# Performance work log

Hardware: AMD Instinct MI355X
Metric: run time of the kernel (lower is better)

The kernel has to match this reference:

```python
import jax, jax.numpy as jnp
import numpy as np

B, C, H, W = 4, 64, 128, 128
EPS = 1e-5


def setup_inputs() -> dict:
    key = jax.random.key(0)
    ks = jax.random.split(key, 6)
    x = jax.random.normal(ks[0], (B, C, H, W), jnp.float32)
    W1 = jax.random.normal(ks[1], (C, C), jnp.float32) * 0.1
    b1 = jnp.zeros((C,), jnp.float32)
    W2 = jax.random.normal(ks[2], (C, C), jnp.float32) * 0.1
    b2 = jnp.zeros((C,), jnp.float32)
    Wc = jax.random.normal(ks[3], (C, C, 3, 3), jnp.float32) * 0.05
    bn_w = jnp.ones((C,), jnp.float32)
    bn_b = jnp.zeros((C,), jnp.float32)
    gamma = jax.random.normal(ks[4], (1,), jnp.float32) * 0.5
    return dict(x=x, W1=W1, b1=b1, W2=W2, b2=b2, Wc=Wc, bn_w=bn_w, bn_b=bn_b, gamma=gamma)


def reference(x, W1, b1, W2, b2, Wc, bn_w, bn_b, gamma):
    b, c, h, w = x.shape
    # feat_h: [B,W,C,H] flattened to [C, B*W, H] (exact torch .view semantics)
    feat_h = x.transpose(0, 3, 1, 2).reshape(c, b * w, h)
    # feat_w: [B,H,C,W] flattened to [C, B*H, W]
    feat_w = x.transpose(0, 2, 1, 3).reshape(c, b * h, w)
    # avg-pool over W -> [B,C,H] -> [C,H,B]; 1x1 conv == channel mix on dim0
    enc_h = jnp.einsum('oi,ihb->ohb', W1, x.mean(axis=3).transpose(1, 2, 0)) + b1[:, None, None]  # [C,H,B]
    enc_w = jnp.einsum('oi,iwb->owb', W2, x.mean(axis=2).transpose(1, 2, 0)) + b2[:, None, None]  # [C,W,B]
    # energy_h: [C, B*W, B*W]
    energy_h = jnp.matmul(feat_h, jnp.tile(enc_h, (1, 1, w)))
    rel_h = jax.nn.softmax(energy_h, axis=-1)
    aug_h = jnp.matmul(rel_h, feat_h).reshape(b, w, c, h).transpose(0, 2, 3, 1)  # [B,C,H,W]
    # energy_w: [C, B*H, B*H]
    energy_w = jnp.matmul(feat_w, jnp.tile(enc_w, (1, 1, h)))
    rel_w = jax.nn.softmax(energy_w, axis=-1)
    aug_w = jnp.matmul(rel_w, feat_w).reshape(b, h, c, w).transpose(0, 2, 1, 3)  # [B,C,H,W]
    out = gamma * (aug_h + aug_w) + x
    # 3x3 conv (no bias) + BatchNorm2d (training-mode batch stats) + ReLU
    y = jax.lax.conv_general_dilated(out, Wc, (1, 1), 'SAME',
                                     dimension_numbers=('NCHW', 'OIHW', 'NCHW'))
    mean = y.mean(axis=(0, 2, 3), keepdims=True)
    var = y.var(axis=(0, 2, 3), keepdims=True)
    y = (y - mean) * jax.lax.rsqrt(var + EPS)
    y = y * bn_w[None, :, None, None] + bn_b[None, :, None, None]
    return jax.nn.relu(y)
```

## Files before the change

kernel.cpp:

```cpp
#include <hip/hip_runtime.h>
#include <math.h>

#define BDIM 4
#define CDIM 64
#define HDIM 128
#define WDIM 128
#define PLANE (HDIM*WDIM)
#define CHW (CDIM*PLANE)

typedef unsigned short ushort_t;
typedef short short8 __attribute__((ext_vector_type(8)));
typedef float floatx4 __attribute__((ext_vector_type(4)));

__device__ inline unsigned int pack_bf16(float lo, float hi) {
  unsigned int ul = __float_as_uint(lo);
  unsigned int uh = __float_as_uint(hi);
  unsigned int rl = (ul + 0x7FFFu + ((ul >> 16) & 1u)) >> 16;
  unsigned int rh = (uh + 0x7FFFu + ((uh >> 16) & 1u)) >> 16;
  return (rh << 16) | (rl & 0xFFFFu);
}

__global__ __launch_bounds__(256) void k1_T_rowmean(const float* __restrict__ x,
                                                    float* __restrict__ T,
                                                    float* __restrict__ xmw) {
  int bid = blockIdx.x;
  int b = bid >> 7, h = bid & 127;
  int t = threadIdx.x;
  int wid = t >> 6, lane = t & 63;
  const float* xp = x + (size_t)b * CHW + h * WDIM;
  float tr[4] = {0,0,0,0}, ur[4] = {0,0,0,0};
#pragma unroll
  for (int cc = 0; cc < 16; cc++) {
    int c = wid * 16 + cc;
    int k = cc & 3;
    float v0 = xp[c * PLANE + lane];
    float v1 = xp[c * PLANE + lane + 64];
    tr[k] += v0; ur[k] += v1;
    float s = v0 + v1;
#pragma unroll
    for (int off = 32; off; off >>= 1) s += __shfl_xor(s, off);
    if (lane == 0) xmw[(b * CDIM + c) * HDIM + h] = s * (1.f / WDIM);
  }
  __shared__ float4 pt[4][128];
  pt[wid][lane]      = make_float4(tr[0], tr[1], tr[2], tr[3]);
  pt[wid][lane + 64] = make_float4(ur[0], ur[1], ur[2], ur[3]);
  __syncthreads();
  if (t < 128) {
    float4 a = pt[0][t], bb = pt[1][t], cvec = pt[2][t], d = pt[3][t];
    float4 s = make_float4(a.x + bb.x + cvec.x + d.x, a.y + bb.y + cvec.y + d.y,
                           a.z + bb.z + cvec.z + d.z, a.w + bb.w + cvec.w + d.w);
    ((float4*)T)[(b * HDIM + h) * WDIM + t] = s;
  }
}

__global__ void k2_colmean(const float* __restrict__ x, float* __restrict__ xmh) {
  int bid = blockIdx.x;
  int b = bid >> 6, c = bid & 63;
  int t = threadIdx.x;
  int tw = t & 127, th2 = t >> 7;
  const float* xp = x + (size_t)(b * CDIM + c) * PLANE;
  float s = 0.f;
  for (int h = th2 * 64; h < th2 * 64 + 64; h++) s += xp[h * WDIM + tw];
  __shared__ float sh[256];
  sh[t] = s;
  __syncthreads();
  if (t < 128) xmh[(b * CDIM + c) * WDIM + t] = (sh[t] + sh[t + 128]) * (1.f / HDIM);
}

__global__ void k3_enc_groups(const float* __restrict__ W1, const float* __restrict__ bias1,
                              const float* __restrict__ W2, const float* __restrict__ bias2,
                              const float* __restrict__ xmw, const float* __restrict__ xmh,
                              const float* __restrict__ T,
                              float* __restrict__ ench, float* __restrict__ encw,
                              float* __restrict__ Gh, float* __restrict__ Gw) {
  int bid = blockIdx.x;
  int t = threadIdx.x;
  if (bid < 256) {
    int o = t >> 2, bb = t & 3;
    if (bid < HDIM) {
      int h = bid;
      float s = bias1[o];
      for (int i = 0; i < CDIM; i++) s += W1[o * CDIM + i] * xmw[(bb * CDIM + i) * HDIM + h];
      ench[(o * HDIM + h) * 4 + bb] = s;
    } else {
      int w = bid - HDIM;
      float s = bias2[o];
      for (int i = 0; i < CDIM; i++) s += W2[o * CDIM + i] * xmh[(bb * CDIM + i) * WDIM + w];
      encw[(o * WDIM + w) * 4 + bb] = s;
    }
  } else if (t < 128) {
    int c2 = bid - 256;
    int b = c2 >> 4;
    int w0 = (c2 & 15) * 8;
    const float4* T4 = (const float4*)T;
    float4 s = make_float4(0, 0, 0, 0);
#pragma unroll
    for (int dw = 0; dw < 8; dw++) {
      float4 v = T4[(b * HDIM + t) * WDIM + w0 + dw];
      s.x += v.x; s.y += v.y; s.z += v.z; s.w += v.w;
    }
    ((float4*)Gh)[c2 * HDIM + t] = s;
    float4 s2 = make_float4(0, 0, 0, 0);
#pragma unroll
    for (int dh = 0; dh < 8; dh++) {
      float4 v = T4[(b * HDIM + w0 + dh) * WDIM + t];
      s2.x += v.x; s2.y += v.y; s2.z += v.z; s2.w += v.w;
    }
    ((float4*)Gw)[c2 * WDIM + t] = s2;
  }
}

__global__ __launch_bounds__(512) void k4_probs(const float* __restrict__ x,
                                                const float* __restrict__ ench,
                                                const float* __restrict__ encw,
                                                float* __restrict__ Ph,
                                                float* __restrict__ Pw) {
  __shared__ float plane[HDIM * WDIM];
  __shared__ float4 esh[512];
  int bid = blockIdx.x;
  int b = bid >> 6, c = bid & 63;
  int t = threadIdx.x;
  const float* xp = x + (size_t)(b * CDIM + c) * PLANE;
#pragma unroll 4
  for (int j = 0; j < 32; j++) {
    int idx = j * 512 + t;
    int row = idx >> 7, col = idx & 127;
    plane[row * WDIM + (col ^ (row & 31))] = xp[idx];
  }
  __syncthreads();
  int q = t >> 7, p = t & 127;
  int branch = q >> 1, seg = q & 1;
  int c2 = (b * HDIM + p) >> 3;
  float e0 = 0, e1 = 0, e2 = 0, e3 = 0;
  if (branch == 0) {
    const float4* E = (const float4*)ench + c2 * HDIM;
    for (int h = seg * 64; h < seg * 64 + 64; h++) {
      float v = plane[h * WDIM + (p ^ (h & 31))];
      float4 e = E[h];
      e0 += v * e.x; e1 += v * e.y; e2 += v * e.z; e3 += v * e.w;
    }
  } else {
    const float4* E = (const float4*)encw + c2 * WDIM;
    for (int w = seg * 64; w < seg * 64 + 64; w++) {
      float v = plane[p * WDIM + (w ^ (p & 31))];
      float4 e = E[w];
      e0 += v * e.x; e1 += v * e.y; e2 += v * e.z; e3 += v * e.w;
    }
  }
  esh[t] = make_float4(e0, e1, e2, e3);
  __syncthreads();
  if (seg == 0) {
    float4 o = esh[t + 128];
    e0 += o.x; e1 += o.y; e2 += o.z; e3 += o.w;
    float m = fmaxf(fmaxf(e0, e1), fmaxf(e2, e3));
    float p0 = __expf(e0 - m), p1 = __expf(e1 - m), p2 = __expf(e2 - m), p3 = __expf(e3 - m);
    float sc = 1.f / ((p0 + p1 + p2 + p3) * 128.f);
    float4* dst = (branch == 0) ? (float4*)Ph : (float4*)Pw;
    dst[c2 * 512 + (p & 7) * 64 + c] = make_float4(p0 * sc, p1 * sc, p2 * sc, p3 * sc);
  }
}

__global__ void k6_prep(const float* __restrict__ Wc, ushort_t* __restrict__ afrag,
                        float* __restrict__ part) {
  int idx = blockIdx.x * 256 + threadIdx.x;
  if (idx < 128) part[idx] = 0.f;
  if (idx >= 4608) return;
  int lane = idx & 63;
  int m = (idx >> 6) & 3;
  int chunk = (idx >> 8) & 1;
  int tap = idx >> 9;
  int dh = tap / 3, dw = tap % 3;
  int o = m * 16 + (lane & 15);
  int ib = chunk * 32 + (lane >> 4) * 8;
  unsigned int d[4];
#pragma unroll
  for (int j = 0; j < 4; j++) {
    float lo = Wc[((size_t)(o * CDIM + ib + 2 * j) * 3 + dh) * 3 + dw];
    float hi = Wc[((size_t)(o * CDIM + ib + 2 * j + 1) * 3 + dh) * 3 + dw];
    d[j] = pack_bf16(lo, hi);
  }
  uint4* dst = (uint4*)afrag + idx;
  *dst = make_uint4(d[0], d[1], d[2], d[3]);
}

__global__ __launch_bounds__(512) void k6_conv(const float* __restrict__ x,
                                               const float* __restrict__ Ph,
                                               const float* __restrict__ Pw,
                                               const float* __restrict__ Gh,
                                               const float* __restrict__ Gw,
                                               const float* __restrict__ gamma,
                                               const ushort_t* __restrict__ afrag,
                                               float* __restrict__ yb,
                                               float* __restrict__ part) {
  __shared__ uint4 lds_in[3 * 130 * 4];
  __shared__ float sh_s[64], sh_ss[64];
  int bid = blockIdx.x;
  int b = bid >> 7, h0 = bid & 127;
  int t = threadIdx.x;
  int lane = t & 63, wv = t >> 6;
  int w0 = wv * 16;
  const float* xb = x + (size_t)b * CHW;
  const float4* Ph4 = (const float4*)Ph;
  const float4* Pw4 = (const float4*)Pw;
  const float4* Gh4 = (const float4*)Gh;
  const float4* Gw4 = (const float4*)Gw;
  float gm = gamma[0];

  if (t < 64) { sh_s[t] = 0.f; sh_ss[t] = 0.f; }

  floatx4 acc[4];
#pragma unroll
  for (int m = 0; m < 4; m++) acc[m] = (floatx4){0.f, 0.f, 0.f, 0.f};

  for (int chunk = 0; chunk < 2; chunk++) {
    int i0 = chunk * 32;
    __syncthreads();
#pragma unroll
    for (int k = 0; k < 4; k++) {
      int gid = k * 512 + t;
      if (gid < 1560) {
        int wlp = gid % 130;
        int rest = gid / 130;
        int g = rest & 3, lr = rest >> 2;
        int h = h0 - 1 + lr, wl = wlp - 1;
        unsigned int d0 = 0, d1 = 0, d2 = 0, d3 = 0;
        if (h >= 0 && h < HDIM && wl >= 0 && wl < WDIM) {
          int c0 = i0 + g * 8;
          int c2h = (b * HDIM + wl) >> 3;
          int c2w = (b * HDIM + h) >> 3;
          float4 gh4 = Gh4[c2h * HDIM + h];
          float4 gw4 = Gw4[c2w * WDIM + wl];
          const float4* php = Ph4 + c2h * 512 + (wl & 7) * 64 + c0;
          const float4* pwp = Pw4 + c2w * 512 + (h & 7) * 64 + c0;
          const float* xpp = xb + (size_t)c0 * PLANE + h * WDIM + wl;
          float v[8];
#pragma unroll
          for (int j = 0; j < 8; j++) {
            float4 ph = php[j], pw = pwp[j];
            float val = ph.x * gh4.x + ph.y * gh4.y + ph.z * gh4.z + ph.w * gh4.w
                      + pw.x * gw4.x + pw.y * gw4.y + pw.z * gw4.z + pw.w * gw4.w;
            v[j] = fmaf(gm, val, xpp[j * PLANE]);
          }
          d0 = pack_bf16(v[0], v[1]); d1 = pack_bf16(v[2], v[3]);
          d2 = pack_bf16(v[4], v[5]); d3 = pack_bf16(v[6], v[7]);
        }
        int pg = g ^ ((wlp >> 1) & 3);
        lds_in[(lr * 130 + wlp) * 4 + pg] = make_uint4(d0, d1, d2, d3);
      }
    }
    __syncthreads();
#pragma unroll
    for (int tap = 0; tap < 9; tap++) {
      int lr = tap / 3, dw = tap % 3;
      int wlp = w0 + (lane & 15) + dw;
      int pg = (lane >> 4) ^ ((wlp >> 1) & 3);
      short8 bf = *(const short8*)&lds_in[(lr * 130 + wlp) * 4 + pg];
      const short8* ap = (const short8*)afrag + (size_t)((tap * 2 + chunk) * 4) * 64 + lane;
#pragma unroll
      for (int m = 0; m < 4; m++) {
        short8 a = ap[m * 64];
        acc[m] = __builtin_amdgcn_mfma_f32_16x16x32_bf16(a, bf, acc[m], 0, 0, 0);
      }
    }
  }
  int col = lane & 15, rg = lane >> 4;
#pragma unroll
  for (int m = 0; m < 4; m++) {
#pragma unroll
    for (int j = 0; j < 4; j++) {
      int o = m * 16 + rg * 4 + j;
      float v = acc[m][j];
      yb[((size_t)(b * CDIM + o) * HDIM + h0) * WDIM + w0 + col] = v;
      float vs = v, vq = v * v;
#pragma unroll
      for (int off = 1; off < 16; off <<= 1) {
        vs += __shfl_xor(vs, off);
        vq += __shfl_xor(vq, off);
      }
      if (col == 0) {
        atomicAdd(&sh_s[o], vs);
        atomicAdd(&sh_ss[o], vq);
      }
    }
  }
  __syncthreads();
  if (t < 64) {
    atomicAdd(&part[t], sh_s[t]);
    atomicAdd(&part[64 + t], sh_ss[t]);
  }
}

__global__ __launch_bounds__(256) void k8_norm(const float* __restrict__ yb,
                                               const float* __restrict__ part,
                                               const float* __restrict__ bnw,
                                               const float* __restrict__ bnb,
                                               float* __restrict__ out) {
  __shared__ float sa[64], sb2[64];
  int t = threadIdx.x;
  if (t < 64) {
    float s = part[t], ss = part[64 + t];
    float m = s * (1.f / 65536.f);
    float var = ss * (1.f / 65536.f) - m * m;
    float a = rsqrtf(var + 1e-5f) * bnw[t];
    sa[t] = a;
    sb2[t] = bnb[t] - m * a;
  }
  __syncthreads();
  int idx = blockIdx.x * 256 + t;
  int c = (idx >> 12) & 63;
  float4 v = ((const float4*)yb)[idx];
  float a = sa[c], bb = sb2[c];
  v.x = fmaxf(0.f, v.x * a + bb);
  v.y = fmaxf(0.f, v.y * a + bb);
  v.z = fmaxf(0.f, v.z * a + bb);
  v.w = fmaxf(0.f, v.w * a + bb);
  ((float4*)out)[idx] = v;
}

extern "C" void kernel_launch(void* const* d_in, const int* in_sizes, int n_in,
                              void* d_out, int out_size, void* d_ws, size_t ws_size,
                              hipStream_t stream) {
  const float* x     = (const float*)d_in[0];
  const float* W1    = (const float*)d_in[1];
  const float* b1    = (const float*)d_in[2];
  const float* W2    = (const float*)d_in[3];
  const float* b2    = (const float*)d_in[4];
  const float* Wc    = (const float*)d_in[5];
  const float* bnw   = (const float*)d_in[6];
  const float* bnb   = (const float*)d_in[7];
  const float* gamma = (const float*)d_in[8];
  float* out = (float*)d_out;

  float* ws   = (float*)d_ws;
  float* T    = ws;
  float* xmw  = T    + 262144;
  float* xmh  = xmw  + 32768;
  float* ench = xmh  + 32768;
  float* encw = ench + 32768;
  float* Ph   = encw + 32768;
  float* Pw   = Ph   + 131072;
  float* Gh   = Pw   + 131072;
  float* Gw   = Gh   + 32768;
  float* yb   = Gw   + 32768;
  float* part = yb   + 4194304;
  ushort_t* afrag = (ushort_t*)(part + 128);

  k6_prep       <<<18, 256, 0, stream>>>(Wc, afrag, part);
  k1_T_rowmean  <<<512, 256, 0, stream>>>(x, T, xmw);
  k2_colmean    <<<256, 256, 0, stream>>>(x, xmh);
  k3_enc_groups <<<320, 256, 0, stream>>>(W1, b1, W2, b2, xmw, xmh, T, ench, encw, Gh, Gw);
  k4_probs      <<<256, 512, 0, stream>>>(x, ench, encw, Ph, Pw);
  k6_conv       <<<512, 512, 0, stream>>>(x, Ph, Pw, Gh, Gw, gamma, afrag, yb, part);
  k8_norm       <<<4096, 256, 0, stream>>>(yb, part, bnw, bnb, out);
}
```

Before: 186.0 us.

## Split conv rows into half-width blocks and stage all channels at once

The conv kernel now uses 1024 blocks of 256 threads, each covering half a row (64 columns), instead of 512 blocks of 512 threads covering full rows. It loads all 64 input channels into LDS in a single pass, with a single barrier instead of two chunked passes. The Ph vectors are loaded once per column and reused across the three halo rows. The goal is more blocks for occupancy and latency hiding and fewer syncs, at the cost of recomputing halo columns at the block edge and a different LDS swizzle.

```diff
diff --git a/kernel.cpp b/kernel.cpp
--- a/kernel.cpp
+++ b/kernel.cpp
@@ -183,22 +183,22 @@
   *dst = make_uint4(d[0], d[1], d[2], d[3]);
 }
 
-__global__ __launch_bounds__(512) void k6_conv(const float* __restrict__ x,
-                                               const float* __restrict__ Ph,
-                                               const float* __restrict__ Pw,
-                                               const float* __restrict__ Gh,
-                                               const float* __restrict__ Gw,
-                                               const float* __restrict__ gamma,
-                                               const ushort_t* __restrict__ afrag,
-                                               float* __restrict__ yb,
-                                               float* __restrict__ part) {
-  __shared__ uint4 lds_in[3 * 130 * 4];
+__global__ __launch_bounds__(256, 4) void k6_conv(const float* __restrict__ x,
+                                                  const float* __restrict__ Ph,
+                                                  const float* __restrict__ Pw,
+                                                  const float* __restrict__ Gh,
+                                                  const float* __restrict__ Gw,
+                                                  const float* __restrict__ gamma,
+                                                  const ushort_t* __restrict__ afrag,
+                                                  float* __restrict__ yb,
+                                                  float* __restrict__ part) {
+  __shared__ uint4 lds_in[3 * 66 * 8];
   __shared__ float sh_s[64], sh_ss[64];
   int bid = blockIdx.x;
-  int b = bid >> 7, h0 = bid & 127;
+  int wb = bid & 1, h0 = (bid >> 1) & 127, b = bid >> 8;
   int t = threadIdx.x;
   int lane = t & 63, wv = t >> 6;
-  int w0 = wv * 16;
+  int wbase = wb * 64;
   const float* xb = x + (size_t)b * CHW;
   const float4* Ph4 = (const float4*)Ph;
   const float4* Pw4 = (const float4*)Pw;
@@ -208,54 +208,60 @@
 
   if (t < 64) { sh_s[t] = 0.f; sh_ss[t] = 0.f; }
 
+  for (int col = t; col < 528; col += 256) {
+    int g = col / 66;
+    int wlp = col - g * 66;
+    int wl = wbase + wlp - 1;
+    int c0 = g * 8;
+    bool wok = (wl >= 0 && wl < WDIM);
+    float4 ph[8];
+    int c2h = 0;
+    if (wok) {
+      c2h = (b * HDIM + wl) >> 3;
+      const float4* php = Ph4 + c2h * 512 + (wl & 7) * 64 + c0;
+#pragma unroll
+      for (int j = 0; j < 8; j++) ph[j] = php[j];
+    }
+    int pg = g ^ (wlp & 7);
+#pragma unroll
+    for (int lr = 0; lr < 3; lr++) {
+      int h = h0 - 1 + lr;
+      unsigned int d0 = 0, d1 = 0, d2 = 0, d3 = 0;
+      if (wok && h >= 0 && h < HDIM) {
+        int c2w = (b * HDIM + h) >> 3;
+        float4 gh4 = Gh4[c2h * HDIM + h];
+        float4 gw4 = Gw4[c2w * WDIM + wl];
+        const float4* pwp = Pw4 + c2w * 512 + (h & 7) * 64 + c0;
+        const float* xpp = xb + (size_t)c0 * PLANE + h * WDIM + wl;
+        float v[8];
+#pragma unroll
+        for (int j = 0; j < 8; j++) {
+          float4 ph4 = ph[j], pw4 = pwp[j];
+          float val = ph4.x * gh4.x + ph4.y * gh4.y + ph4.z * gh4.z + ph4.w * gh4.w
+                    + pw4.x * gw4.x + pw4.y * gw4.y + pw4.z * gw4.z + pw4.w * gw4.w;
+          v[j] = fmaf(gm, val, xpp[j * PLANE]);
+        }
+        d0 = pack_bf16(v[0], v[1]); d1 = pack_bf16(v[2], v[3]);
+        d2 = pack_bf16(v[4], v[5]); d3 = pack_bf16(v[6], v[7]);
+      }
+      lds_in[(lr * 66 + wlp) * 8 + pg] = make_uint4(d0, d1, d2, d3);
+    }
+  }
+  __syncthreads();
+
   floatx4 acc[4];
 #pragma unroll
   for (int m = 0; m < 4; m++) acc[m] = (floatx4){0.f, 0.f, 0.f, 0.f};
-
-  for (int chunk = 0; chunk < 2; chunk++) {
-    int i0 = chunk * 32;
-    __syncthreads();
-#pragma unroll
-    for (int k = 0; k < 4; k++) {
-      int gid = k * 512 + t;
-      if (gid < 1560) {
-        int wlp = gid % 130;
-        int rest = gid / 130;
-        int g = rest & 3, lr = rest >> 2;
-        int h = h0 - 1 + lr, wl = wlp - 1;
-        unsigned int d0 = 0, d1 = 0, d2 = 0, d3 = 0;
-        if (h >= 0 && h < HDIM && wl >= 0 && wl < WDIM) {
-          int c0 = i0 + g * 8;
-          int c2h = (b * HDIM + wl) >> 3;
-          int c2w = (b * HDIM + h) >> 3;
-          float4 gh4 = Gh4[c2h * HDIM + h];
-          float4 gw4 = Gw4[c2w * WDIM + wl];
-          const float4* php = Ph4 + c2h * 512 + (wl & 7) * 64 + c0;
-          const float4* pwp = Pw4 + c2w * 512 + (h & 7) * 64 + c0;
-          const float* xpp = xb + (size_t)c0 * PLANE + h * WDIM + wl;
-          float v[8];
-#pragma unroll
-          for (int j = 0; j < 8; j++) {
-            float4 ph = php[j], pw = pwp[j];
-            float val = ph.x * gh4.x + ph.y * gh4.y + ph.z * gh4.z + ph.w * gh4.w
-                      + pw.x * gw4.x + pw.y * gw4.y + pw.z * gw4.z + pw.w * gw4.w;
-            v[j] = fmaf(gm, val, xpp[j * PLANE]);
-          }
-          d0 = pack_bf16(v[0], v[1]); d1 = pack_bf16(v[2], v[3]);
-          d2 = pack_bf16(v[4], v[5]); d3 = pack_bf16(v[6], v[7]);
-        }
-        int pg = g ^ ((wlp >> 1) & 3);
-        lds_in[(lr * 130 + wlp) * 4 + pg] = make_uint4(d0, d1, d2, d3);
-      }
-    }
-    __syncthreads();
-#pragma unroll
-    for (int tap = 0; tap < 9; tap++) {
-      int lr = tap / 3, dw = tap % 3;
-      int wlp = w0 + (lane & 15) + dw;
-      int pg = (lane >> 4) ^ ((wlp >> 1) & 3);
-      short8 bf = *(const short8*)&lds_in[(lr * 130 + wlp) * 4 + pg];
-      const short8* ap = (const short8*)afrag + (size_t)((tap * 2 + chunk) * 4) * 64 + lane;
+  int w0loc = wv * 16;
+#pragma unroll
+  for (int tap = 0; tap < 9; tap++) {
+    int lr = tap / 3, dw = tap % 3;
+    int wlp = w0loc + (lane & 15) + dw;
+#pragma unroll
+    for (int kc = 0; kc < 2; kc++) {
+      int pg = (kc * 4 + (lane >> 4)) ^ (wlp & 7);
+      short8 bf = *(const short8*)&lds_in[(lr * 66 + wlp) * 8 + pg];
+      const short8* ap = (const short8*)afrag + (size_t)((tap * 2 + kc) * 4) * 64 + lane;
 #pragma unroll
       for (int m = 0; m < 4; m++) {
         short8 a = ap[m * 64];
@@ -263,6 +269,7 @@
       }
     }
   }
+
   int col = lane & 15, rg = lane >> 4;
 #pragma unroll
   for (int m = 0; m < 4; m++) {
@@ -270,7 +277,7 @@
     for (int j = 0; j < 4; j++) {
       int o = m * 16 + rg * 4 + j;
       float v = acc[m][j];
-      yb[((size_t)(b * CDIM + o) * HDIM + h0) * WDIM + w0 + col] = v;
+      yb[((size_t)(b * CDIM + o) * HDIM + h0) * WDIM + wbase + w0loc + col] = v;
       float vs = v, vq = v * v;
 #pragma unroll
       for (int off = 1; off < 16; off <<= 1) {
@@ -350,6 +357,6 @@
   k2_colmean    <<<256, 256, 0, stream>>>(x, xmh);
   k3_enc_groups <<<320, 256, 0, stream>>>(W1, b1, W2, b2, xmw, xmh, T, ench, encw, Gh, Gw);
   k4_probs      <<<256, 512, 0, stream>>>(x, ench, encw, Ph, Pw);
-  k6_conv       <<<512, 512, 0, stream>>>(x, Ph, Pw, Gh, Gw, gamma, afrag, yb, part);
+  k6_conv       <<<1024, 256, 0, stream>>>(x, Ph, Pw, Gh, Gw, gamma, afrag, yb, part);
   k8_norm       <<<4096, 256, 0, stream>>>(yb, part, bnw, bnb, out);
 }
```

Result: no change. 187.9 us (+1.0%).
